# Optimization experiments

Hardware: AMD Instinct MI355X
Metric: run time of the kernel (lower is better)

Reference implementation:

```python
import jax, jax.numpy as jnp
import numpy as np


def _binarize_ste(t):
    # torch code overwrites .data with sign(), which acts as a straight-through
    # identity for autograd: forward = sign(t), backward = identity.
    return t + jax.lax.stop_gradient(jnp.sign(t) - t)


def setup_inputs() -> dict:
    key = jax.random.key(0)
    k1, k2 = jax.random.split(key)
    B, C_IN, C_OUT = 512, 1536, 512
    x = jax.random.normal(k1, (B, C_IN), dtype=jnp.float32)
    stdv = 1.0 / np.sqrt(C_OUT * C_IN)
    weight = jax.random.uniform(k2, (C_OUT, C_IN), dtype=jnp.float32,
                                minval=-stdv, maxval=stdv)
    return {"x": x, "weight": weight}


def reference(x, weight):
    B, c_in = x.shape
    c_out = weight.shape[0]
    G = c_in // 3  # majority-3 group count
    bx = _binarize_ste(x)        # [B, c_in] in {-1, 0, +1}
    bw = _binarize_ste(weight)   # [c_out, c_in]
    # einsum('bj,cj->bcj') then group-sum over triples == contract only within
    # each group of 3, never materializing the full [B, c_out, c_in] tensor.
    inter = jnp.einsum('bgk,cgk->bcg',
                       bx.reshape(B, G, 3),
                       bw.reshape(c_out, G, 3))  # [B, c_out, G]
    out = 2.25 * jnp.sum(jnp.clip(inter, -1.0, 1.0), axis=-1)  # [B, c_out]
    return out
```

## Files before the change

### kernel.cpp

```cpp
#include <hip/hip_runtime.h>
#include <hip/hip_bf16.h>
#include <stdint.h>


#define CIN    1536
#define B_DIM  512
#define COUT   512
#define WORDS3 52
#define WSTRIDE 54

__global__ __launch_bounds__(256) void pack_kernel(
    const float* __restrict__ x, const float* __restrict__ w,
    uint2* __restrict__ px, uint2* __restrict__ pw) {
  __shared__ float buf[CIN];
  const int bid = blockIdx.x;
  const float* src;
  uint2* dst;
  if (bid < 512) { src = x + (size_t)bid * CIN;        dst = px + (size_t)bid * WORDS3; }
  else           { src = w + (size_t)(bid - 512) * CIN; dst = pw + (size_t)(bid - 512) * WORDS3; }

  const float4* s4 = (const float4*)src;
  float4* b4 = (float4*)buf;
  #pragma unroll
  for (int i = threadIdx.x; i < CIN / 4; i += 256) b4[i] = s4[i];
  __syncthreads();

  const int wd = threadIdx.x;
  if (wd < WORDS3) {
    const float* rowp = buf + wd * 30;
    int nmax = CIN - wd * 30;
    unsigned P = 0, N = 0;
    #pragma unroll
    for (int k = 0; k < 30; k++) {
      if (k < nmax) {
        float v = rowp[k];
        P |= (v > 0.0f ? 1u : 0u) << k;
        N |= (v < 0.0f ? 1u : 0u) << k;
      }
    }
    dst[wd] = make_uint2(P, N);
  }
}

__device__ __forceinline__ void maj3w(unsigned xp, unsigned xn,
                                      unsigned wp, unsigned wn,
                                      int& gt, int& ge) {
  const unsigned M1 = 0x09249249u;
  const unsigned M4 = 0x24924924u;
  unsigned pos = (xp & wp) | (xn & wn);
  unsigned neg = (xp & wn) | (xn & wp);
  unsigned cp = (pos & M1) + ((pos >> 1) & M1) + ((pos >> 2) & M1);
  unsigned cn = (neg & M1) + ((neg >> 1) & M1) + ((neg >> 2) & M1);
  unsigned u = (cp | M4) - cn;
  unsigned t = u - M1;
  gt += __popc(t & M4);
  ge += __popc(u & M4);
}

__global__ __launch_bounds__(256) void maj3_kernel(
    const uint2* __restrict__ px, const uint2* __restrict__ pw,
    float* __restrict__ out) {
  __shared__ __align__(16) uint2 sx[16][WSTRIDE];
  __shared__ __align__(16) uint2 sw[8][WSTRIDE];
  __shared__ int comb[128];

  const int b0 = blockIdx.y * 16;
  const int c0 = blockIdx.x * 8;
  const int tid = threadIdx.x;

  const uint4* gx = (const uint4*)(px + (size_t)b0 * WORDS3);
  const uint4* gw = (const uint4*)(pw + (size_t)c0 * WORDS3);
  uint4* lx = (uint4*)sx;
  uint4* lw = (uint4*)sw;
  #pragma unroll
  for (int i = tid; i < 16 * 26; i += 256) {
    int r = i / 26, wd = i - r * 26;
    lx[r * 27 + wd] = gx[i];
  }
  if (tid < 8 * 26) {
    int r = tid / 26, wd = tid - r * 26;
    lw[r * 27 + wd] = gw[tid];
  }
  __syncthreads();

  const int o  = tid & 127;
  const int tx = o & 7;
  const int ty = o >> 3;
  const int h  = tid >> 7;

  const uint4* xr = (const uint4*)&sx[ty][0];
  const uint4* wr = (const uint4*)&sw[tx][0];
  const int hb = h * 13;

  int gt0 = 0, ge0 = 0, gt1 = 0, ge1 = 0;

  uint4 x0 = xr[hb],     w0 = wr[hb];
  uint4 x1 = xr[hb + 1], w1 = wr[hb + 1];
  #pragma unroll
  for (int i = 0; i < 13; i++) {
    uint4 xa = x0, wb = w0;
    x0 = x1; w0 = w1;
    int nx = (i + 2 < 13) ? (hb + i + 2) : hb;
    x1 = xr[nx]; w1 = wr[nx];
    maj3w(xa.x, xa.y, wb.x, wb.y, gt0, ge0);
    maj3w(xa.z, xa.w, wb.z, wb.w, gt1, ge1);
  }

  int partial = gt0 + ge0 + gt1 + ge1;
  if (h == 1) comb[o] = partial;
  __syncthreads();
  if (h == 0) {
    int total = partial + comb[o];
    out[(size_t)(b0 + ty) * COUT + (c0 + tx)] = 2.25f * (float)(total - 520);
  }
}

extern "C" void kernel_launch(void* const* d_in, const int* in_sizes, int n_in,
                              void* d_out, int out_size, void* d_ws, size_t ws_size,
                              hipStream_t stream) {
  const float* x = (const float*)d_in[0];
  const float* w = (const float*)d_in[1];
  float* out = (float*)d_out;

  uint2* px = (uint2*)d_ws;
  uint2* pw = px + (size_t)B_DIM * WORDS3;

  pack_kernel<<<1024, 256, 0, stream>>>(x, w, px, pw);

  dim3 grid(COUT / 8, B_DIM / 16);
  maj3_kernel<<<grid, 256, 0, stream>>>(px, pw, out);
}
```

Baseline: 69.97 us.

## Pack bit-planes per group position and use full-adder majority logic

The packing changes from 10 groups per 30-bit word to a bit-sliced layout with three planes per sign polarity, holding 32 groups per word set. The pack kernel now runs one thread per 96-float slice, reading directly from global memory with no shared staging, over 64 blocks. The main kernel evaluates majority-of-three with full-adder boolean logic across 32 groups per step, cutting per-group instructions and wasted bits. Occupancy launch bounds are also raised. The pack kernel now has far fewer threads, each loading 384 bytes, which may lower memory parallelism for that stage.

```diff
diff --git a/kernel.cpp b/kernel.cpp
--- a/kernel.cpp
+++ b/kernel.cpp
@@ -1,85 +1,95 @@
 #include <hip/hip_runtime.h>
-#include <hip/hip_bf16.h>
 #include <stdint.h>
 
 
-#define CIN    1536
-#define B_DIM  512
-#define COUT   512
-#define WORDS3 52
-#define WSTRIDE 54
+#define CIN     1536
+#define B_DIM   512
+#define COUT    512
+#define GROUPS  512
+#define ROW_U4  24
+#define XSTRIDE 25
 
 __global__ __launch_bounds__(256) void pack_kernel(
     const float* __restrict__ x, const float* __restrict__ w,
-    uint2* __restrict__ px, uint2* __restrict__ pw) {
-  __shared__ float buf[CIN];
-  const int bid = blockIdx.x;
-  const float* src;
-  uint2* dst;
-  if (bid < 512) { src = x + (size_t)bid * CIN;        dst = px + (size_t)bid * WORDS3; }
-  else           { src = w + (size_t)(bid - 512) * CIN; dst = pw + (size_t)(bid - 512) * WORDS3; }
+    uint32_t* __restrict__ packed) {
+  const int t = blockIdx.x * 256 + threadIdx.x;
+  const int row = t >> 4;
+  const int slice = t & 15;
+  const float* src = (row < B_DIM) ? (x + (size_t)row * CIN)
+                                   : (w + (size_t)(row - B_DIM) * CIN);
+  const float4* s4 = (const float4*)(src + slice * 96);
 
-  const float4* s4 = (const float4*)src;
-  float4* b4 = (float4*)buf;
+  unsigned P0 = 0, P1 = 0, P2 = 0, N0 = 0, N1 = 0, N2 = 0;
   #pragma unroll
-  for (int i = threadIdx.x; i < CIN / 4; i += 256) b4[i] = s4[i];
-  __syncthreads();
-
-  const int wd = threadIdx.x;
-  if (wd < WORDS3) {
-    const float* rowp = buf + wd * 30;
-    int nmax = CIN - wd * 30;
-    unsigned P = 0, N = 0;
+  for (int i = 0; i < 8; i++) {
+    float4 q0 = s4[3 * i], q1 = s4[3 * i + 1], q2 = s4[3 * i + 2];
+    float f[12] = {q0.x, q0.y, q0.z, q0.w, q1.x, q1.y, q1.z, q1.w,
+                   q2.x, q2.y, q2.z, q2.w};
     #pragma unroll
-    for (int k = 0; k < 30; k++) {
-      if (k < nmax) {
-        float v = rowp[k];
-        P |= (v > 0.0f ? 1u : 0u) << k;
-        N |= (v < 0.0f ? 1u : 0u) << k;
-      }
+    for (int g = 0; g < 4; g++) {
+      const int bit = i * 4 + g;
+      float a = f[3 * g], b = f[3 * g + 1], c = f[3 * g + 2];
+      P0 |= (a > 0.0f ? 1u : 0u) << bit;
+      N0 |= (a < 0.0f ? 1u : 0u) << bit;
+      P1 |= (b > 0.0f ? 1u : 0u) << bit;
+      N1 |= (b < 0.0f ? 1u : 0u) << bit;
+      P2 |= (c > 0.0f ? 1u : 0u) << bit;
+      N2 |= (c < 0.0f ? 1u : 0u) << bit;
     }
-    dst[wd] = make_uint2(P, N);
   }
+  uint32_t* dst = packed + (size_t)row * 96 + (slice >> 1) * 12 + (slice & 1);
+  dst[0] = P0;  dst[2] = P1;  dst[4]  = P2;
+  dst[6] = N0;  dst[8] = N1;  dst[10] = N2;
 }
 
-__device__ __forceinline__ void maj3w(unsigned xp, unsigned xn,
-                                      unsigned wp, unsigned wn,
-                                      int& gt, int& ge) {
-  const unsigned M1 = 0x09249249u;
-  const unsigned M4 = 0x24924924u;
-  unsigned pos = (xp & wp) | (xn & wn);
-  unsigned neg = (xp & wn) | (xn & wp);
-  unsigned cp = (pos & M1) + ((pos >> 1) & M1) + ((pos >> 2) & M1);
-  unsigned cn = (neg & M1) + ((neg >> 1) & M1) + ((neg >> 2) & M1);
-  unsigned u = (cp | M4) - cn;
-  unsigned t = u - M1;
-  gt += __popc(t & M4);
-  ge += __popc(u & M4);
+__device__ __forceinline__ void maj32(
+    unsigned xp0, unsigned xp1, unsigned xp2,
+    unsigned xn0, unsigned xn1, unsigned xn2,
+    unsigned wp0, unsigned wp1, unsigned wp2,
+    unsigned wn0, unsigned wn1, unsigned wn2,
+    int& acc) {
+  unsigned pos0 = (xp0 & wp0) | (xn0 & wn0);
+  unsigned pos1 = (xp1 & wp1) | (xn1 & wn1);
+  unsigned pos2 = (xp2 & wp2) | (xn2 & wn2);
+  unsigned neg0 = (xp0 & wn0) | (xn0 & wp0);
+  unsigned neg1 = (xp1 & wn1) | (xn1 & wp1);
+  unsigned neg2 = (xp2 & wn2) | (xn2 & wp2);
+  unsigned sa  = pos0 ^ pos1;
+  unsigned cp0 = sa ^ pos2;
+  unsigned cp1 = (pos0 & pos1) | (pos2 & sa);
+  unsigned sb  = neg0 ^ neg1;
+  unsigned cn0 = sb ^ neg2;
+  unsigned cn1 = (neg0 & neg1) | (neg2 & sb);
+  unsigned nh = ~cn1;
+  unsigned nl = ~cn0;
+  unsigned hi = cp1 & nh;
+  unsigned eq = ~(cp1 ^ cn1);
+  unsigned gt = hi | (eq & (cp0 & nl));
+  unsigned ge = hi | (eq & (cp0 | nl));
+  acc += __popc(gt) + __popc(ge);
 }
 
-__global__ __launch_bounds__(256) void maj3_kernel(
-    const uint2* __restrict__ px, const uint2* __restrict__ pw,
+__global__ __launch_bounds__(256, 8) void maj3_kernel(
+    const uint4* __restrict__ px, const uint4* __restrict__ pw,
     float* __restrict__ out) {
-  __shared__ __align__(16) uint2 sx[16][WSTRIDE];
-  __shared__ __align__(16) uint2 sw[8][WSTRIDE];
+  __shared__ __align__(16) uint4 sx[16][XSTRIDE];
+  __shared__ __align__(16) uint4 sw[8][XSTRIDE];
   __shared__ int comb[128];
 
   const int b0 = blockIdx.y * 16;
   const int c0 = blockIdx.x * 8;
   const int tid = threadIdx.x;
 
-  const uint4* gx = (const uint4*)(px + (size_t)b0 * WORDS3);
-  const uint4* gw = (const uint4*)(pw + (size_t)c0 * WORDS3);
-  uint4* lx = (uint4*)sx;
-  uint4* lw = (uint4*)sw;
+  const uint4* gx = px + (size_t)b0 * ROW_U4;
+  const uint4* gw = pw + (size_t)c0 * ROW_U4;
   #pragma unroll
-  for (int i = tid; i < 16 * 26; i += 256) {
-    int r = i / 26, wd = i - r * 26;
-    lx[r * 27 + wd] = gx[i];
+  for (int i = tid; i < 16 * ROW_U4; i += 256) {
+    int r = i / ROW_U4, wd = i - r * ROW_U4;
+    sx[r][wd] = gx[i];
   }
-  if (tid < 8 * 26) {
-    int r = tid / 26, wd = tid - r * 26;
-    lw[r * 27 + wd] = gw[tid];
+  if (tid < 8 * ROW_U4) {
+    int r = tid / ROW_U4, wd = tid - r * ROW_U4;
+    sw[r][wd] = gw[tid];
   }
   __syncthreads();
 
@@ -88,30 +98,25 @@
   const int ty = o >> 3;
   const int h  = tid >> 7;
 
-  const uint4* xr = (const uint4*)&sx[ty][0];
-  const uint4* wr = (const uint4*)&sw[tx][0];
-  const int hb = h * 13;
+  const uint4* xr = &sx[ty][h * 12];
+  const uint4* wr = &sw[tx][h * 12];
 
-  int gt0 = 0, ge0 = 0, gt1 = 0, ge1 = 0;
-
-  uint4 x0 = xr[hb],     w0 = wr[hb];
-  uint4 x1 = xr[hb + 1], w1 = wr[hb + 1];
+  int acc = 0;
   #pragma unroll
-  for (int i = 0; i < 13; i++) {
-    uint4 xa = x0, wb = w0;
-    x0 = x1; w0 = w1;
-    int nx = (i + 2 < 13) ? (hb + i + 2) : hb;
-    x1 = xr[nx]; w1 = wr[nx];
-    maj3w(xa.x, xa.y, wb.x, wb.y, gt0, ge0);
-    maj3w(xa.z, xa.w, wb.z, wb.w, gt1, ge1);
+  for (int i = 0; i < 4; i++) {
+    uint4 a0 = xr[3 * i], a1 = xr[3 * i + 1], a2 = xr[3 * i + 2];
+    uint4 b0v = wr[3 * i], b1 = wr[3 * i + 1], b2 = wr[3 * i + 2];
+    maj32(a0.x, a0.z, a1.x, a1.z, a2.x, a2.z,
+          b0v.x, b0v.z, b1.x, b1.z, b2.x, b2.z, acc);
+    maj32(a0.y, a0.w, a1.y, a1.w, a2.y, a2.w,
+          b0v.y, b0v.w, b1.y, b1.w, b2.y, b2.w, acc);
   }
 
-  int partial = gt0 + ge0 + gt1 + ge1;
-  if (h == 1) comb[o] = partial;
+  if (h == 1) comb[o] = acc;
   __syncthreads();
   if (h == 0) {
-    int total = partial + comb[o];
-    out[(size_t)(b0 + ty) * COUT + (c0 + tx)] = 2.25f * (float)(total - 520);
+    int total = acc + comb[o];
+    out[(size_t)(b0 + ty) * COUT + (c0 + tx)] = 2.25f * (float)(total - GROUPS);
   }
 }
 
@@ -122,10 +127,11 @@
   const float* w = (const float*)d_in[1];
   float* out = (float*)d_out;
 
-  uint2* px = (uint2*)d_ws;
-  uint2* pw = px + (size_t)B_DIM * WORDS3;
+  uint32_t* packed = (uint32_t*)d_ws;
+  const uint4* px = (const uint4*)packed;
+  const uint4* pw = (const uint4*)(packed + (size_t)B_DIM * 96);
 
-  pack_kernel<<<1024, 256, 0, stream>>>(x, w, px, pw);
+  pack_kernel<<<64, 256, 0, stream>>>(x, w, packed);
 
   dim3 grid(COUT / 8, B_DIM / 16);
   maj3_kernel<<<grid, 256, 0, stream>>>(px, pw, out);
```

Result: faster. 66.52 us (-4.9%).
